# Kernel optimization log

Hardware: AMD Instinct MI355X
Metric: run time of the kernel (lower is better)

The kernel has to match this reference:

```python
import jax, jax.numpy as jnp
import numpy as np


def _phi(z, conv_w, conv_b):
    # z: (H, W, S, 1) -> 3x3 SAME conv over state channels -> softmax over states
    x = jnp.transpose(z[..., 0], (2, 0, 1))[None]  # (1, S, H, W)
    y = jax.lax.conv_general_dilated(
        x, conv_w, window_strides=(1, 1), padding='SAME',
        dimension_numbers=('NCHW', 'OIHW', 'NCHW')) + conv_b[None, :, None, None]
    return jax.nn.softmax(jnp.transpose(y[0], (1, 2, 0)), axis=2)[..., None]  # (H, W, S, 1)


def _update(obs, P, u_k, w_k_O, conv_w, conv_b):
    H, W, O = obs.shape
    S = P.shape[0]
    # b = P^T @ obs per cell: b[h,w,s] = sum_o P[o,s] * obs[h,w,o]
    b = jnp.einsum('os,hwo->hws', P, obs)[..., None]  # (H, W, S, 1)
    # Analytic Jacobian db/dP: deriv_b[h,w,s,0,i,j] = obs[h,w,i] * delta(s==j)
    eye = jnp.eye(S, O, dtype=obs.dtype)
    deriv_b = (obs[:, :, None, :, None] * eye[None, None, :, None, :])[:, :, :, None, :, :]  # (H,W,S,1,S,O)

    Bu = b * u_k                                  # (H, W, S, 1)
    bu = jnp.sum(Bu, axis=2, keepdims=True)       # (H, W, 1, 1)
    Z = Bu / bu                                   # Bu / bu

    u_kp1 = _phi(Z, conv_w, conv_b)               # (H, W, S, 1)

    # Sensitivity recursion for obs params (quotient rule on Bu/bu)
    du = deriv_b * u_k[..., None, None] + b[..., None, None] * w_k_O  # (H,W,S,1,S,O)
    term1 = du * bu[..., None, None]
    term2 = jnp.expand_dims(jnp.sum(du, axis=2), 3) * Bu[..., None, None]
    w_pre = (term1 - term2) / bu[..., None, None] ** 2                # (H,W,S,1,S,O)

    # J @ w  ==  9 JVPs of Phi at Z with tangent columns of w (exact, avoids dense (HWS)^2 Jacobian)
    tangents = jnp.moveaxis(w_pre.reshape(H, W, S, 1, S * O), -1, 0)  # (S*O, H, W, S, 1)
    jvp1 = lambda t: jax.jvp(lambda z: _phi(z, conv_w, conv_b), (Z,), (t,))[1]
    w_kp1_O = jnp.moveaxis(jax.vmap(jvp1)(tangents), 0, -1).reshape(H, W, S, 1, S, O)
    return u_kp1, w_kp1_O


def setup_inputs() -> dict:
    key = jax.random.key(0)
    k1, k2, k3 = jax.random.split(key, 3)
    H = W = 512
    S = O = 3
    obs = jax.random.uniform(k1, (H, W, O), dtype=jnp.float32)
    obs_param_matrix = jnp.ones((S, O), jnp.float32) / O          # row-stochastic init
    u_k = jnp.ones((H, W, S, 1), jnp.float32) / S                 # uniform belief
    w_k_O = jnp.zeros((H, W, S, 1, S, O), jnp.float32)
    conv_w = jax.random.normal(k2, (S, S, 3, 3), jnp.float32) * 0.1
    conv_b = jax.random.normal(k3, (S,), jnp.float32) * 0.1
    return {'obs': obs, 'obs_param_matrix': obs_param_matrix, 'u_k': u_k,
            'w_k_O': w_k_O, 'conv_w': conv_w, 'conv_b': conv_b}


def reference(obs, obs_param_matrix, u_k, w_k_O, conv_w, conv_b):
    return _update(obs, obs_param_matrix, u_k, w_k_O, conv_w, conv_b)
```

## Files before the change

kernel.cpp:

```cpp
#include <hip/hip_runtime.h>

#define IMH 512
#define IMW 512
#define TW 16
#define TH 16
#define HW_ (TW + 2)
#define HH_ (TH + 2)
#define NHALO (HW_ * HH_)
#define ROW 31

typedef float f4 __attribute__((ext_vector_type(4)));
typedef float f4a __attribute__((ext_vector_type(4), aligned(4)));
typedef float f2a __attribute__((ext_vector_type(2), aligned(4)));

__global__ __launch_bounds__(256, 4)
void hmm_fused(const float* __restrict__ obs,
               const float* __restrict__ P,
               const float* __restrict__ u_k,
               const float* __restrict__ w_k,
               const float* __restrict__ conv_w,
               const float* __restrict__ conv_b,
               float* __restrict__ out) {
    __shared__ __align__(16) float lds[NHALO * ROW];

    const int tid = threadIdx.x;
    const int w0 = blockIdx.x * TW;
    const int h0 = blockIdx.y * TH;

    float Pm[9];
#pragma unroll
    for (int i = 0; i < 9; ++i) Pm[i] = P[i];

    for (int p = tid; p < NHALO; p += 256) {
        const int hh = h0 + p / HW_ - 1;
        const int ww = w0 + p % HW_ - 1;
        float* row = &lds[p * ROW];
        if (hh < 0 || hh >= IMH || ww < 0 || ww >= IMW) {
#pragma unroll
            for (int c = 0; c < 30; ++c) row[c] = 0.0f;
            continue;
        }
        const int pix = hh * IMW + ww;

        const f2a o01 = *(const f2a*)(obs + pix * 3);
        const float o2 = obs[pix * 3 + 2];
        const f2a u01 = *(const f2a*)(u_k + pix * 3);
        const float u2 = u_k[pix * 3 + 2];
        const float ov[3] = {o01.x, o01.y, o2};
        const float us[3] = {u01.x, u01.y, u2};

        const float* wkp = &w_k[(size_t)pix * 27];
        float wreg[27];
        {
            const f4a* v4 = (const f4a*)wkp;
            const f4a a0 = v4[0], a1 = v4[1], a2 = v4[2], a3 = v4[3], a4 = v4[4], a5 = v4[5];
            const f2a a6 = *(const f2a*)(wkp + 24);
            const float a7 = wkp[26];
            wreg[0] = a0.x;  wreg[1] = a0.y;  wreg[2] = a0.z;  wreg[3] = a0.w;
            wreg[4] = a1.x;  wreg[5] = a1.y;  wreg[6] = a1.z;  wreg[7] = a1.w;
            wreg[8] = a2.x;  wreg[9] = a2.y;  wreg[10] = a2.z; wreg[11] = a2.w;
            wreg[12] = a3.x; wreg[13] = a3.y; wreg[14] = a3.z; wreg[15] = a3.w;
            wreg[16] = a4.x; wreg[17] = a4.y; wreg[18] = a4.z; wreg[19] = a4.w;
            wreg[20] = a5.x; wreg[21] = a5.y; wreg[22] = a5.z; wreg[23] = a5.w;
            wreg[24] = a6.x; wreg[25] = a6.y; wreg[26] = a7;
        }

        float b[3], Bu[3], bu = 0.0f;
#pragma unroll
        for (int s = 0; s < 3; ++s) {
            b[s] = Pm[0 * 3 + s] * ov[0] + Pm[1 * 3 + s] * ov[1] + Pm[2 * 3 + s] * ov[2];
            Bu[s] = b[s] * us[s];
            bu += Bu[s];
        }
        const float inv_bu = 1.0f / bu;
        float Z[3];
#pragma unroll
        for (int s = 0; s < 3; ++s) { Z[s] = Bu[s] * inv_bu; row[s] = Z[s]; }

#pragma unroll
        for (int i = 0; i < 3; ++i) {
#pragma unroll
            for (int j = 0; j < 3; ++j) {
                const int ij = i * 3 + j;
                float du[3], sdu = 0.0f;
#pragma unroll
                for (int s = 0; s < 3; ++s) {
                    float d = b[s] * wreg[s * 9 + ij];
                    if (s == j) d += ov[i] * us[s];
                    du[s] = d;
                    sdu += d;
                }
#pragma unroll
                for (int s = 0; s < 3; ++s)
                    row[(1 + ij) * 3 + s] = (du[s] - sdu * Z[s]) * inv_bu;
            }
        }
    }

    float cw[81];
#pragma unroll
    for (int i = 0; i < 81; ++i) cw[i] = conv_w[i];
    const float cb[3] = {conv_b[0], conv_b[1], conv_b[2]};

    __syncthreads();

    const int tx = tid % TW, ty = tid / TW;
    const int hp = (ty + 1) * HW_ + (tx + 1);
    const int pix = (h0 + ty) * IMW + (w0 + tx);

    float p0, p1, p2;
    {
        float y[3] = {cb[0], cb[1], cb[2]};
#pragma unroll
        for (int ky = 0; ky < 3; ++ky) {
#pragma unroll
            for (int kx = 0; kx < 3; ++kx) {
                const float* nb = &lds[(hp + (ky - 1) * HW_ + (kx - 1)) * ROW];
                const float v0 = nb[0], v1 = nb[1], v2 = nb[2];
#pragma unroll
                for (int s = 0; s < 3; ++s)
                    y[s] += cw[s * 27 + 0 * 9 + ky * 3 + kx] * v0 +
                            cw[s * 27 + 1 * 9 + ky * 3 + kx] * v1 +
                            cw[s * 27 + 2 * 9 + ky * 3 + kx] * v2;
            }
        }
        const float m = fmaxf(y[0], fmaxf(y[1], y[2]));
        const float e0 = __expf(y[0] - m), e1 = __expf(y[1] - m), e2 = __expf(y[2] - m);
        const float inv = 1.0f / (e0 + e1 + e2);
        p0 = e0 * inv; p1 = e1 * inv; p2 = e2 * inv;
        out[pix * 3 + 0] = p0; out[pix * 3 + 1] = p1; out[pix * 3 + 2] = p2;
    }

    float wout[27];
#pragma unroll
    for (int g = 1; g < 10; ++g) {
        float a[3] = {0.0f, 0.0f, 0.0f};
#pragma unroll
        for (int ky = 0; ky < 3; ++ky) {
#pragma unroll
            for (int kx = 0; kx < 3; ++kx) {
                const float* nb = &lds[(hp + (ky - 1) * HW_ + (kx - 1)) * ROW];
                const float v0 = nb[g * 3 + 0], v1 = nb[g * 3 + 1], v2 = nb[g * 3 + 2];
#pragma unroll
                for (int s = 0; s < 3; ++s)
                    a[s] += cw[s * 27 + 0 * 9 + ky * 3 + kx] * v0 +
                            cw[s * 27 + 1 * 9 + ky * 3 + kx] * v1 +
                            cw[s * 27 + 2 * 9 + ky * 3 + kx] * v2;
            }
        }
        const float dot = p0 * a[0] + p1 * a[1] + p2 * a[2];
        const int ij = g - 1;
        wout[0 * 9 + ij] = p0 * (a[0] - dot);
        wout[1 * 9 + ij] = p0 * 0.0f + p0 * (a[0] - dot);
        wout[0 * 9 + ij] = p0 * (a[0] - dot);
        wout[1 * 9 + ij] = p1 * (a[1] - dot);
        wout[2 * 9 + ij] = p2 * (a[2] - dot);
    }

    __syncthreads();

#pragma unroll
    for (int c = 0; c < 27; ++c) lds[tid * 27 + c] = wout[c];
    __syncthreads();

    const f4* lds4 = (const f4*)lds;
    float* outw = out + IMH * IMW * 3;
    for (int idx = tid; idx < TW * TH * 27 / 4; idx += 256) {
        const int r = idx / 108;
        const int rem = idx - r * 108;
        *(f4*)(&outw[(h0 + r) * (IMW * 27) + w0 * 27 + rem * 4]) = lds4[idx];
    }
}

extern "C" void kernel_launch(void* const* d_in, const int* in_sizes, int n_in,
                              void* d_out, int out_size, void* d_ws, size_t ws_size,
                              hipStream_t stream) {
    const float* obs    = (const float*)d_in[0];
    const float* P      = (const float*)d_in[1];
    const float* u_k    = (const float*)d_in[2];
    const float* w_k    = (const float*)d_in[3];
    const float* conv_w = (const float*)d_in[4];
    const float* conv_b = (const float*)d_in[5];
    float* out = (float*)d_out;

    dim3 grid(IMW / TW, IMH / TH);
    hmm_fused<<<grid, 256, 0, stream>>>(obs, P, u_k, w_k, conv_w, conv_b, out);
}
```

Before: 118.3 us.

## Halve tile height and split per-pixel tangent columns across two threads

Tiles shrink from 16x16 to 16x8 pixels while blocks keep 256 threads. The halo (180 cells) is now computed with one cell per thread, with no loop. For the second conv, two threads share each pixel: one handles 4 of the 9 tangent columns and the other handles 5. Both threads recompute the softmax. This halves LDS use and the per-thread register arrays, and the launch bound rises to 6 blocks per CU so occupancy and the number of blocks can grow. The costs are a larger halo-to-interior ratio, redundant softmax work, and an uneven 4/5 split between the two halves.

```diff
diff --git a/kernel.cpp b/kernel.cpp
--- a/kernel.cpp
+++ b/kernel.cpp
@@ -3,17 +3,18 @@
 #define IMH 512
 #define IMW 512
 #define TW 16
-#define TH 16
+#define TH 8
 #define HW_ (TW + 2)
 #define HH_ (TH + 2)
 #define NHALO (HW_ * HH_)
+#define NPIX (TW * TH)
 #define ROW 31
 
 typedef float f4 __attribute__((ext_vector_type(4)));
 typedef float f4a __attribute__((ext_vector_type(4), aligned(4)));
 typedef float f2a __attribute__((ext_vector_type(2), aligned(4)));
 
-__global__ __launch_bounds__(256, 4)
+__global__ __launch_bounds__(256, 6)
 void hmm_fused(const float* __restrict__ obs,
                const float* __restrict__ P,
                const float* __restrict__ u_k,
@@ -31,68 +32,69 @@
 #pragma unroll
     for (int i = 0; i < 9; ++i) Pm[i] = P[i];
 
-    for (int p = tid; p < NHALO; p += 256) {
+    if (tid < NHALO) {
+        const int p = tid;
         const int hh = h0 + p / HW_ - 1;
         const int ww = w0 + p % HW_ - 1;
         float* row = &lds[p * ROW];
         if (hh < 0 || hh >= IMH || ww < 0 || ww >= IMW) {
 #pragma unroll
             for (int c = 0; c < 30; ++c) row[c] = 0.0f;
-            continue;
-        }
-        const int pix = hh * IMW + ww;
+        } else {
+            const int pix = hh * IMW + ww;
 
-        const f2a o01 = *(const f2a*)(obs + pix * 3);
-        const float o2 = obs[pix * 3 + 2];
-        const f2a u01 = *(const f2a*)(u_k + pix * 3);
-        const float u2 = u_k[pix * 3 + 2];
-        const float ov[3] = {o01.x, o01.y, o2};
-        const float us[3] = {u01.x, u01.y, u2};
+            const f2a o01 = *(const f2a*)(obs + pix * 3);
+            const float o2 = obs[pix * 3 + 2];
+            const f2a u01 = *(const f2a*)(u_k + pix * 3);
+            const float u2 = u_k[pix * 3 + 2];
+            const float ov[3] = {o01.x, o01.y, o2};
+            const float us[3] = {u01.x, u01.y, u2};
 
-        const float* wkp = &w_k[(size_t)pix * 27];
-        float wreg[27];
-        {
-            const f4a* v4 = (const f4a*)wkp;
-            const f4a a0 = v4[0], a1 = v4[1], a2 = v4[2], a3 = v4[3], a4 = v4[4], a5 = v4[5];
-            const f2a a6 = *(const f2a*)(wkp + 24);
-            const float a7 = wkp[26];
-            wreg[0] = a0.x;  wreg[1] = a0.y;  wreg[2] = a0.z;  wreg[3] = a0.w;
-            wreg[4] = a1.x;  wreg[5] = a1.y;  wreg[6] = a1.z;  wreg[7] = a1.w;
-            wreg[8] = a2.x;  wreg[9] = a2.y;  wreg[10] = a2.z; wreg[11] = a2.w;
-            wreg[12] = a3.x; wreg[13] = a3.y; wreg[14] = a3.z; wreg[15] = a3.w;
-            wreg[16] = a4.x; wreg[17] = a4.y; wreg[18] = a4.z; wreg[19] = a4.w;
-            wreg[20] = a5.x; wreg[21] = a5.y; wreg[22] = a5.z; wreg[23] = a5.w;
-            wreg[24] = a6.x; wreg[25] = a6.y; wreg[26] = a7;
-        }
+            const float* wkp = &w_k[(size_t)pix * 27];
+            float wreg[27];
+            {
+                const f4a* v4 = (const f4a*)wkp;
+                const f4a a0 = v4[0], a1 = v4[1], a2 = v4[2], a3 = v4[3], a4 = v4[4], a5 = v4[5];
+                const f2a a6 = *(const f2a*)(wkp + 24);
+                const float a7 = wkp[26];
+                wreg[0] = a0.x;  wreg[1] = a0.y;  wreg[2] = a0.z;  wreg[3] = a0.w;
+                wreg[4] = a1.x;  wreg[5] = a1.y;  wreg[6] = a1.z;  wreg[7] = a1.w;
+                wreg[8] = a2.x;  wreg[9] = a2.y;  wreg[10] = a2.z; wreg[11] = a2.w;
+                wreg[12] = a3.x; wreg[13] = a3.y; wreg[14] = a3.z; wreg[15] = a3.w;
+                wreg[16] = a4.x; wreg[17] = a4.y; wreg[18] = a4.z; wreg[19] = a4.w;
+                wreg[20] = a5.x; wreg[21] = a5.y; wreg[22] = a5.z; wreg[23] = a5.w;
+                wreg[24] = a6.x; wreg[25] = a6.y; wreg[26] = a7;
+            }
 
-        float b[3], Bu[3], bu = 0.0f;
+            float b[3], Bu[3], bu = 0.0f;
 #pragma unroll
-        for (int s = 0; s < 3; ++s) {
-            b[s] = Pm[0 * 3 + s] * ov[0] + Pm[1 * 3 + s] * ov[1] + Pm[2 * 3 + s] * ov[2];
-            Bu[s] = b[s] * us[s];
-            bu += Bu[s];
-        }
-        const float inv_bu = 1.0f / bu;
-        float Z[3];
+            for (int s = 0; s < 3; ++s) {
+                b[s] = Pm[0 * 3 + s] * ov[0] + Pm[1 * 3 + s] * ov[1] + Pm[2 * 3 + s] * ov[2];
+                Bu[s] = b[s] * us[s];
+                bu += Bu[s];
+            }
+            const float inv_bu = 1.0f / bu;
+            float Z[3];
 #pragma unroll
-        for (int s = 0; s < 3; ++s) { Z[s] = Bu[s] * inv_bu; row[s] = Z[s]; }
+            for (int s = 0; s < 3; ++s) { Z[s] = Bu[s] * inv_bu; row[s] = Z[s]; }
 
 #pragma unroll
-        for (int i = 0; i < 3; ++i) {
+            for (int i = 0; i < 3; ++i) {
 #pragma unroll
-            for (int j = 0; j < 3; ++j) {
-                const int ij = i * 3 + j;
-                float du[3], sdu = 0.0f;
+                for (int j = 0; j < 3; ++j) {
+                    const int ij = i * 3 + j;
+                    float du[3], sdu = 0.0f;
 #pragma unroll
-                for (int s = 0; s < 3; ++s) {
-                    float d = b[s] * wreg[s * 9 + ij];
-                    if (s == j) d += ov[i] * us[s];
-                    du[s] = d;
-                    sdu += d;
+                    for (int s = 0; s < 3; ++s) {
+                        float d = b[s] * wreg[s * 9 + ij];
+                        if (s == j) d += ov[i] * us[s];
+                        du[s] = d;
+                        sdu += d;
+                    }
+#pragma unroll
+                    for (int s = 0; s < 3; ++s)
+                        row[(1 + ij) * 3 + s] = (du[s] - sdu * Z[s]) * inv_bu;
                 }
-#pragma unroll
-                for (int s = 0; s < 3; ++s)
-                    row[(1 + ij) * 3 + s] = (du[s] - sdu * Z[s]) * inv_bu;
             }
         }
     }
@@ -104,7 +106,9 @@
 
     __syncthreads();
 
-    const int tx = tid % TW, ty = tid / TW;
+    const int half = tid >> 7;
+    const int pxl = tid & 127;
+    const int tx = pxl & 15, ty = pxl >> 4;
     const int hp = (ty + 1) * HW_ + (tx + 1);
     const int pix = (h0 + ty) * IMW + (w0 + tx);
 
@@ -128,12 +132,16 @@
         const float e0 = __expf(y[0] - m), e1 = __expf(y[1] - m), e2 = __expf(y[2] - m);
         const float inv = 1.0f / (e0 + e1 + e2);
         p0 = e0 * inv; p1 = e1 * inv; p2 = e2 * inv;
-        out[pix * 3 + 0] = p0; out[pix * 3 + 1] = p1; out[pix * 3 + 2] = p2;
+        if (half == 0) { out[pix * 3 + 0] = p0; out[pix * 3 + 1] = p1; out[pix * 3 + 2] = p2; }
     }
 
-    float wout[27];
+    const int ij0 = half ? 4 : 0;
+    const int ng  = half ? 5 : 4;
+    float wout[5][3];
 #pragma unroll
-    for (int g = 1; g < 10; ++g) {
+    for (int k = 0; k < 5; ++k) {
+        if (k >= ng) break;
+        const int g = ij0 + k + 1;
         float a[3] = {0.0f, 0.0f, 0.0f};
 #pragma unroll
         for (int ky = 0; ky < 3; ++ky) {
@@ -149,23 +157,25 @@
             }
         }
         const float dot = p0 * a[0] + p1 * a[1] + p2 * a[2];
-        const int ij = g - 1;
-        wout[0 * 9 + ij] = p0 * (a[0] - dot);
-        wout[1 * 9 + ij] = p0 * 0.0f + p0 * (a[0] - dot);
-        wout[0 * 9 + ij] = p0 * (a[0] - dot);
-        wout[1 * 9 + ij] = p1 * (a[1] - dot);
-        wout[2 * 9 + ij] = p2 * (a[2] - dot);
+        wout[k][0] = p0 * (a[0] - dot);
+        wout[k][1] = p1 * (a[1] - dot);
+        wout[k][2] = p2 * (a[2] - dot);
     }
 
     __syncthreads();
 
 #pragma unroll
-    for (int c = 0; c < 27; ++c) lds[tid * 27 + c] = wout[c];
+    for (int k = 0; k < 5; ++k) {
+        if (k >= ng) break;
+        const int ij = ij0 + k;
+#pragma unroll
+        for (int s = 0; s < 3; ++s) lds[pxl * 27 + s * 9 + ij] = wout[k][s];
+    }
     __syncthreads();
 
     const f4* lds4 = (const f4*)lds;
     float* outw = out + IMH * IMW * 3;
-    for (int idx = tid; idx < TW * TH * 27 / 4; idx += 256) {
+    for (int idx = tid; idx < NPIX * 27 / 4; idx += 256) {
         const int r = idx / 108;
         const int rem = idx - r * 108;
         *(f4*)(&outw[(h0 + r) * (IMW * 27) + w0 * 27 + rem * 4]) = lds4[idx];
```

Result: slower. 145.9 us (+23.3%).

## Halve tile height and redistribute tangent convolution across threads by channel group

Applied to the files above, without the earlier changes.

Tile height drops to 8, so each 256-thread block loads its 180-pixel halo in a single pass. Softmax probabilities go to shared memory, and the nine tangent-channel convolutions are spread over 144 threads. Each of these threads owns one column and one channel group, sweeps down the rows with a rolling three-row accumulator, and writes results straight to global memory. This removes the per-thread 27-output serial loop and the LDS staging pass for output. In exchange, the output writes are strided rather than coalesced float4, and many threads sit idle in some phases.

```diff
diff --git a/kernel.cpp b/kernel.cpp
--- a/kernel.cpp
+++ b/kernel.cpp
@@ -3,10 +3,11 @@
 #define IMH 512
 #define IMW 512
 #define TW 16
-#define TH 16
+#define TH 8
 #define HW_ (TW + 2)
 #define HH_ (TH + 2)
 #define NHALO (HW_ * HH_)
+#define NPIX (TW * TH)
 #define ROW 31
 
 typedef float f4 __attribute__((ext_vector_type(4)));
@@ -22,6 +23,7 @@
                const float* __restrict__ conv_b,
                float* __restrict__ out) {
     __shared__ __align__(16) float lds[NHALO * ROW];
+    __shared__ f4 p_aux4[NPIX];
 
     const int tid = threadIdx.x;
     const int w0 = blockIdx.x * TW;
@@ -31,68 +33,69 @@
 #pragma unroll
     for (int i = 0; i < 9; ++i) Pm[i] = P[i];
 
-    for (int p = tid; p < NHALO; p += 256) {
+    if (tid < NHALO) {
+        const int p = tid;
         const int hh = h0 + p / HW_ - 1;
         const int ww = w0 + p % HW_ - 1;
         float* row = &lds[p * ROW];
         if (hh < 0 || hh >= IMH || ww < 0 || ww >= IMW) {
 #pragma unroll
             for (int c = 0; c < 30; ++c) row[c] = 0.0f;
-            continue;
-        }
-        const int pix = hh * IMW + ww;
-
-        const f2a o01 = *(const f2a*)(obs + pix * 3);
-        const float o2 = obs[pix * 3 + 2];
-        const f2a u01 = *(const f2a*)(u_k + pix * 3);
-        const float u2 = u_k[pix * 3 + 2];
-        const float ov[3] = {o01.x, o01.y, o2};
-        const float us[3] = {u01.x, u01.y, u2};
-
-        const float* wkp = &w_k[(size_t)pix * 27];
-        float wreg[27];
-        {
-            const f4a* v4 = (const f4a*)wkp;
-            const f4a a0 = v4[0], a1 = v4[1], a2 = v4[2], a3 = v4[3], a4 = v4[4], a5 = v4[5];
-            const f2a a6 = *(const f2a*)(wkp + 24);
-            const float a7 = wkp[26];
-            wreg[0] = a0.x;  wreg[1] = a0.y;  wreg[2] = a0.z;  wreg[3] = a0.w;
-            wreg[4] = a1.x;  wreg[5] = a1.y;  wreg[6] = a1.z;  wreg[7] = a1.w;
-            wreg[8] = a2.x;  wreg[9] = a2.y;  wreg[10] = a2.z; wreg[11] = a2.w;
-            wreg[12] = a3.x; wreg[13] = a3.y; wreg[14] = a3.z; wreg[15] = a3.w;
-            wreg[16] = a4.x; wreg[17] = a4.y; wreg[18] = a4.z; wreg[19] = a4.w;
-            wreg[20] = a5.x; wreg[21] = a5.y; wreg[22] = a5.z; wreg[23] = a5.w;
-            wreg[24] = a6.x; wreg[25] = a6.y; wreg[26] = a7;
-        }
-
-        float b[3], Bu[3], bu = 0.0f;
-#pragma unroll
-        for (int s = 0; s < 3; ++s) {
-            b[s] = Pm[0 * 3 + s] * ov[0] + Pm[1 * 3 + s] * ov[1] + Pm[2 * 3 + s] * ov[2];
-            Bu[s] = b[s] * us[s];
-            bu += Bu[s];
-        }
-        const float inv_bu = 1.0f / bu;
-        float Z[3];
-#pragma unroll
-        for (int s = 0; s < 3; ++s) { Z[s] = Bu[s] * inv_bu; row[s] = Z[s]; }
-
-#pragma unroll
-        for (int i = 0; i < 3; ++i) {
-#pragma unroll
-            for (int j = 0; j < 3; ++j) {
-                const int ij = i * 3 + j;
-                float du[3], sdu = 0.0f;
-#pragma unroll
-                for (int s = 0; s < 3; ++s) {
-                    float d = b[s] * wreg[s * 9 + ij];
-                    if (s == j) d += ov[i] * us[s];
-                    du[s] = d;
-                    sdu += d;
+        } else {
+            const int pix = hh * IMW + ww;
+
+            const f2a o01 = *(const f2a*)(obs + pix * 3);
+            const float o2 = obs[pix * 3 + 2];
+            const f2a u01 = *(const f2a*)(u_k + pix * 3);
+            const float u2 = u_k[pix * 3 + 2];
+            const float ov[3] = {o01.x, o01.y, o2};
+            const float us[3] = {u01.x, u01.y, u2};
+
+            const float* wkp = &w_k[(size_t)pix * 27];
+            float wreg[27];
+            {
+                const f4a* v4 = (const f4a*)wkp;
+                const f4a a0 = v4[0], a1 = v4[1], a2 = v4[2], a3 = v4[3], a4 = v4[4], a5 = v4[5];
+                const f2a a6 = *(const f2a*)(wkp + 24);
+                const float a7 = wkp[26];
+                wreg[0] = a0.x;  wreg[1] = a0.y;  wreg[2] = a0.z;  wreg[3] = a0.w;
+                wreg[4] = a1.x;  wreg[5] = a1.y;  wreg[6] = a1.z;  wreg[7] = a1.w;
+                wreg[8] = a2.x;  wreg[9] = a2.y;  wreg[10] = a2.z; wreg[11] = a2.w;
+                wreg[12] = a3.x; wreg[13] = a3.y; wreg[14] = a3.z; wreg[15] = a3.w;
+                wreg[16] = a4.x; wreg[17] = a4.y; wreg[18] = a4.z; wreg[19] = a4.w;
+                wreg[20] = a5.x; wreg[21] = a5.y; wreg[22] = a5.z; wreg[23] = a5.w;
+                wreg[24] = a6.x; wreg[25] = a6.y; wreg[26] = a7;
+            }
+
+            float b[3], Bu[3], bu = 0.0f;
+#pragma unroll
+            for (int s = 0; s < 3; ++s) {
+                b[s] = Pm[0 * 3 + s] * ov[0] + Pm[1 * 3 + s] * ov[1] + Pm[2 * 3 + s] * ov[2];
+                Bu[s] = b[s] * us[s];
+                bu += Bu[s];
+            }
+            const float inv_bu = 1.0f / bu;
+            float Z[3];
+#pragma unroll
+            for (int s = 0; s < 3; ++s) { Z[s] = Bu[s] * inv_bu; row[s] = Z[s]; }
+
+#pragma unroll
+            for (int i = 0; i < 3; ++i) {
+#pragma unroll
+                for (int j = 0; j < 3; ++j) {
+                    const int ij = i * 3 + j;
+                    float du[3], sdu = 0.0f;
+#pragma unroll
+                    for (int s = 0; s < 3; ++s) {
+                        float d = b[s] * wreg[s * 9 + ij];
+                        if (s == j) d += ov[i] * us[s];
+                        du[s] = d;
+                        sdu += d;
+                    }
+#pragma unroll
+                    for (int s = 0; s < 3; ++s)
+                        row[(1 + ij) * 3 + s] = (du[s] - sdu * Z[s]) * inv_bu;
                 }
-#pragma unroll
-                for (int s = 0; s < 3; ++s)
-                    row[(1 + ij) * 3 + s] = (du[s] - sdu * Z[s]) * inv_bu;
             }
         }
     }
@@ -100,75 +103,91 @@
     float cw[81];
 #pragma unroll
     for (int i = 0; i < 81; ++i) cw[i] = conv_w[i];
-    const float cb[3] = {conv_b[0], conv_b[1], conv_b[2]};
+    const float cb0 = conv_b[0], cb1 = conv_b[1], cb2 = conv_b[2];
 
     __syncthreads();
 
-    const int tx = tid % TW, ty = tid / TW;
-    const int hp = (ty + 1) * HW_ + (tx + 1);
-    const int pix = (h0 + ty) * IMW + (w0 + tx);
-
-    float p0, p1, p2;
-    {
-        float y[3] = {cb[0], cb[1], cb[2]};
+    float* outw = out + IMH * IMW * 3;
+
+    if (tid < NPIX) {
+        const int tx = tid & 15, ty = tid >> 4;
+        const int hp = (ty + 1) * HW_ + (tx + 1);
+        const int pix = (h0 + ty) * IMW + (w0 + tx);
+        float y0 = cb0, y1 = cb1, y2 = cb2;
 #pragma unroll
         for (int ky = 0; ky < 3; ++ky) {
 #pragma unroll
             for (int kx = 0; kx < 3; ++kx) {
                 const float* nb = &lds[(hp + (ky - 1) * HW_ + (kx - 1)) * ROW];
                 const float v0 = nb[0], v1 = nb[1], v2 = nb[2];
-#pragma unroll
-                for (int s = 0; s < 3; ++s)
-                    y[s] += cw[s * 27 + 0 * 9 + ky * 3 + kx] * v0 +
-                            cw[s * 27 + 1 * 9 + ky * 3 + kx] * v1 +
-                            cw[s * 27 + 2 * 9 + ky * 3 + kx] * v2;
+                const int T = ky * 3 + kx;
+                y0 += cw[0 + T] * v0 + cw[9 + T] * v1 + cw[18 + T] * v2;
+                y1 += cw[27 + T] * v0 + cw[36 + T] * v1 + cw[45 + T] * v2;
+                y2 += cw[54 + T] * v0 + cw[63 + T] * v1 + cw[72 + T] * v2;
             }
         }
-        const float m = fmaxf(y[0], fmaxf(y[1], y[2]));
-        const float e0 = __expf(y[0] - m), e1 = __expf(y[1] - m), e2 = __expf(y[2] - m);
+        const float m = fmaxf(y0, fmaxf(y1, y2));
+        const float e0 = __expf(y0 - m), e1 = __expf(y1 - m), e2 = __expf(y2 - m);
         const float inv = 1.0f / (e0 + e1 + e2);
-        p0 = e0 * inv; p1 = e1 * inv; p2 = e2 * inv;
+        const float p0 = e0 * inv, p1 = e1 * inv, p2 = e2 * inv;
         out[pix * 3 + 0] = p0; out[pix * 3 + 1] = p1; out[pix * 3 + 2] = p2;
+        p_aux4[tid] = (f4){p0, p1, p2, 0.0f};
     }
 
-    float wout[27];
-#pragma unroll
-    for (int g = 1; g < 10; ++g) {
-        float a[3] = {0.0f, 0.0f, 0.0f};
-#pragma unroll
-        for (int ky = 0; ky < 3; ++ky) {
-#pragma unroll
-            for (int kx = 0; kx < 3; ++kx) {
-                const float* nb = &lds[(hp + (ky - 1) * HW_ + (kx - 1)) * ROW];
-                const float v0 = nb[g * 3 + 0], v1 = nb[g * 3 + 1], v2 = nb[g * 3 + 2];
-#pragma unroll
-                for (int s = 0; s < 3; ++s)
-                    a[s] += cw[s * 27 + 0 * 9 + ky * 3 + kx] * v0 +
-                            cw[s * 27 + 1 * 9 + ky * 3 + kx] * v1 +
-                            cw[s * 27 + 2 * 9 + ky * 3 + kx] * v2;
-            }
-        }
-        const float dot = p0 * a[0] + p1 * a[1] + p2 * a[2];
+    __syncthreads();
+
+    if (tid < 144) {
+        const int x = tid & 15;
+        const int g = (tid >> 4) + 1;
         const int ij = g - 1;
-        wout[0 * 9 + ij] = p0 * (a[0] - dot);
-        wout[1 * 9 + ij] = p0 * 0.0f + p0 * (a[0] - dot);
-        wout[0 * 9 + ij] = p0 * (a[0] - dot);
-        wout[1 * 9 + ij] = p1 * (a[1] - dot);
-        wout[2 * 9 + ij] = p2 * (a[2] - dot);
-    }
-
-    __syncthreads();
-
-#pragma unroll
-    for (int c = 0; c < 27; ++c) lds[tid * 27 + c] = wout[c];
-    __syncthreads();
-
-    const f4* lds4 = (const f4*)lds;
-    float* outw = out + IMH * IMW * 3;
-    for (int idx = tid; idx < TW * TH * 27 / 4; idx += 256) {
-        const int r = idx / 108;
-        const int rem = idx - r * 108;
-        *(f4*)(&outw[(h0 + r) * (IMW * 27) + w0 * 27 + rem * 4]) = lds4[idx];
+        const int gch = 3 * g;
+
+        float a00, a01, a02;
+        float b10, b11, b12;
+        float c20, c21, c22;
+
+#define ROWFMA(P0_, P1_, P2_, KY)                                                        \
+        P0_ += cw[0 + (KY)*3 + 0] * v00 + cw[9 + (KY)*3 + 0] * v01 + cw[18 + (KY)*3 + 0] * v02; \
+        P1_ += cw[27 + (KY)*3 + 0] * v00 + cw[36 + (KY)*3 + 0] * v01 + cw[45 + (KY)*3 + 0] * v02; \
+        P2_ += cw[54 + (KY)*3 + 0] * v00 + cw[63 + (KY)*3 + 0] * v01 + cw[72 + (KY)*3 + 0] * v02; \
+        P0_ += cw[0 + (KY)*3 + 1] * v10 + cw[9 + (KY)*3 + 1] * v11 + cw[18 + (KY)*3 + 1] * v12; \
+        P1_ += cw[27 + (KY)*3 + 1] * v10 + cw[36 + (KY)*3 + 1] * v11 + cw[45 + (KY)*3 + 1] * v12; \
+        P2_ += cw[54 + (KY)*3 + 1] * v10 + cw[63 + (KY)*3 + 1] * v11 + cw[72 + (KY)*3 + 1] * v12; \
+        P0_ += cw[0 + (KY)*3 + 2] * v20 + cw[9 + (KY)*3 + 2] * v21 + cw[18 + (KY)*3 + 2] * v22; \
+        P1_ += cw[27 + (KY)*3 + 2] * v20 + cw[36 + (KY)*3 + 2] * v21 + cw[45 + (KY)*3 + 2] * v22; \
+        P2_ += cw[54 + (KY)*3 + 2] * v20 + cw[63 + (KY)*3 + 2] * v21 + cw[72 + (KY)*3 + 2] * v22;
+
+#define FINISH(O, Q0, Q1, Q2) {                                                          \
+        const f4 pv = p_aux4[(O) * 16 + x];                                              \
+        const float dot_ = pv.x * (Q0) + pv.y * (Q1) + pv.z * (Q2);                      \
+        float* wp = outw + ((size_t)((h0 + (O)) * IMW + (w0 + x))) * 27 + ij;            \
+        wp[0]  = pv.x * ((Q0) - dot_);                                                   \
+        wp[9]  = pv.y * ((Q1) - dot_);                                                   \
+        wp[18] = pv.z * ((Q2) - dot_); }
+
+#define STEP(R, N0,N1,N2, M0,M1,M2, O0,O1,O2, DO_N, DO_M, DO_O) {                        \
+        const int rb = ((R) * HW_ + x) * ROW + gch;                                      \
+        const float v00 = lds[rb + 0],  v01 = lds[rb + 1],  v02 = lds[rb + 2];           \
+        const float v10 = lds[rb + 31], v11 = lds[rb + 32], v12 = lds[rb + 33];          \
+        const float v20 = lds[rb + 62], v21 = lds[rb + 63], v22 = lds[rb + 64];          \
+        if (DO_N) { N0 = 0.0f; N1 = 0.0f; N2 = 0.0f; ROWFMA(N0, N1, N2, 0) }             \
+        if (DO_M) { ROWFMA(M0, M1, M2, 1) }                                              \
+        if (DO_O) { ROWFMA(O0, O1, O2, 2) FINISH((R) - 2, O0, O1, O2) } }
+
+        STEP(0, a00,a01,a02, b10,b11,b12, c20,c21,c22, true,  false, false)
+        STEP(1, b10,b11,b12, a00,a01,a02, c20,c21,c22, true,  true,  false)
+        STEP(2, c20,c21,c22, b10,b11,b12, a00,a01,a02, true,  true,  true )
+        STEP(3, a00,a01,a02, c20,c21,c22, b10,b11,b12, true,  true,  true )
+        STEP(4, b10,b11,b12, a00,a01,a02, c20,c21,c22, true,  true,  true )
+        STEP(5, c20,c21,c22, b10,b11,b12, a00,a01,a02, true,  true,  true )
+        STEP(6, a00,a01,a02, c20,c21,c22, b10,b11,b12, true,  true,  true )
+        STEP(7, b10,b11,b12, a00,a01,a02, c20,c21,c22, true,  true,  true )
+        STEP(8, c20,c21,c22, b10,b11,b12, a00,a01,a02, false, true,  true )
+        STEP(9, a00,a01,a02, c20,c21,c22, b10,b11,b12, false, false, true )
+
+#undef STEP
+#undef FINISH
+#undef ROWFMA
     }
 }
 
```

After: 105.6 us. -10.8%, faster.

## Split fused kernel into two stages via padded channel-planar workspace

Applied to the files above, without the earlier changes.

Replaces the single tiled kernel, which staged a haloed 30-channel tile in LDS, with two kernels. The first writes Z and the nine tangent groups into a zero-padded, channel-planar global workspace. The second reads 3x3 neighbourhoods straight from global memory and splits the nine JVP groups across two half-blocks. This removes LDS pressure, the halo recomputation and the barriers, at the cost of an extra round trip of about 30 MB through global memory and uncoalesced stride-27 output stores.

```diff
diff --git a/kernel.cpp b/kernel.cpp
--- a/kernel.cpp
+++ b/kernel.cpp
@@ -2,174 +2,155 @@
 
 #define IMH 512
 #define IMW 512
-#define TW 16
-#define TH 16
-#define HW_ (TW + 2)
-#define HH_ (TH + 2)
-#define NHALO (HW_ * HH_)
-#define ROW 31
+#define PW 514
+#define PS (PW * PW)
+#define NCH 30
+#define UOFF (IMH * IMW * 3)
 
-typedef float f4 __attribute__((ext_vector_type(4)));
 typedef float f4a __attribute__((ext_vector_type(4), aligned(4)));
 typedef float f2a __attribute__((ext_vector_type(2), aligned(4)));
 
+
 __global__ __launch_bounds__(256, 4)
-void hmm_fused(const float* __restrict__ obs,
-               const float* __restrict__ P,
-               const float* __restrict__ u_k,
-               const float* __restrict__ w_k,
-               const float* __restrict__ conv_w,
-               const float* __restrict__ conv_b,
-               float* __restrict__ out) {
-    __shared__ __align__(16) float lds[NHALO * ROW];
+void hmm_stage_a(const float* __restrict__ obs,
+                 const float* __restrict__ P,
+                 const float* __restrict__ u_k,
+                 const float* __restrict__ w_k,
+                 float* __restrict__ ws) {
+    const int cell = blockIdx.x * 256 + threadIdx.x;
+    if (cell >= PS) return;
+    const int y = cell / PW;
+    const int x = cell - y * PW;
 
-    const int tid = threadIdx.x;
-    const int w0 = blockIdx.x * TW;
-    const int h0 = blockIdx.y * TH;
+    if (y == 0 || y == PW - 1 || x == 0 || x == PW - 1) {
+#pragma unroll
+        for (int c = 0; c < NCH; ++c) ws[c * PS + cell] = 0.0f;
+        return;
+    }
 
     float Pm[9];
 #pragma unroll
     for (int i = 0; i < 9; ++i) Pm[i] = P[i];
 
-    for (int p = tid; p < NHALO; p += 256) {
-        const int hh = h0 + p / HW_ - 1;
-        const int ww = w0 + p % HW_ - 1;
-        float* row = &lds[p * ROW];
-        if (hh < 0 || hh >= IMH || ww < 0 || ww >= IMW) {
+    const int pix = (y - 1) * IMW + (x - 1);
+
+    const f2a o01 = *(const f2a*)(obs + pix * 3);
+    const float o2 = obs[pix * 3 + 2];
+    const f2a u01 = *(const f2a*)(u_k + pix * 3);
+    const float u2 = u_k[pix * 3 + 2];
+    const float ov[3] = {o01.x, o01.y, o2};
+    const float us[3] = {u01.x, u01.y, u2};
+
+    const float* wkp = &w_k[(size_t)pix * 27];
+    float wreg[27];
+    {
+        const f4a* v4 = (const f4a*)wkp;
+        const f4a a0 = v4[0], a1 = v4[1], a2 = v4[2], a3 = v4[3], a4 = v4[4], a5 = v4[5];
+        const f2a a6 = *(const f2a*)(wkp + 24);
+        const float a7 = wkp[26];
+        wreg[0] = a0.x;  wreg[1] = a0.y;  wreg[2] = a0.z;  wreg[3] = a0.w;
+        wreg[4] = a1.x;  wreg[5] = a1.y;  wreg[6] = a1.z;  wreg[7] = a1.w;
+        wreg[8] = a2.x;  wreg[9] = a2.y;  wreg[10] = a2.z; wreg[11] = a2.w;
+        wreg[12] = a3.x; wreg[13] = a3.y; wreg[14] = a3.z; wreg[15] = a3.w;
+        wreg[16] = a4.x; wreg[17] = a4.y; wreg[18] = a4.z; wreg[19] = a4.w;
+        wreg[20] = a5.x; wreg[21] = a5.y; wreg[22] = a5.z; wreg[23] = a5.w;
+        wreg[24] = a6.x; wreg[25] = a6.y; wreg[26] = a7;
+    }
+
+    float b[3], Bu[3], bu = 0.0f;
 #pragma unroll
-            for (int c = 0; c < 30; ++c) row[c] = 0.0f;
-            continue;
-        }
-        const int pix = hh * IMW + ww;
-
-        const f2a o01 = *(const f2a*)(obs + pix * 3);
-        const float o2 = obs[pix * 3 + 2];
-        const f2a u01 = *(const f2a*)(u_k + pix * 3);
-        const float u2 = u_k[pix * 3 + 2];
-        const float ov[3] = {o01.x, o01.y, o2};
-        const float us[3] = {u01.x, u01.y, u2};
-
-        const float* wkp = &w_k[(size_t)pix * 27];
-        float wreg[27];
-        {
-            const f4a* v4 = (const f4a*)wkp;
-            const f4a a0 = v4[0], a1 = v4[1], a2 = v4[2], a3 = v4[3], a4 = v4[4], a5 = v4[5];
-            const f2a a6 = *(const f2a*)(wkp + 24);
-            const float a7 = wkp[26];
-            wreg[0] = a0.x;  wreg[1] = a0.y;  wreg[2] = a0.z;  wreg[3] = a0.w;
-            wreg[4] = a1.x;  wreg[5] = a1.y;  wreg[6] = a1.z;  wreg[7] = a1.w;
-            wreg[8] = a2.x;  wreg[9] = a2.y;  wreg[10] = a2.z; wreg[11] = a2.w;
-            wreg[12] = a3.x; wreg[13] = a3.y; wreg[14] = a3.z; wreg[15] = a3.w;
-            wreg[16] = a4.x; wreg[17] = a4.y; wreg[18] = a4.z; wreg[19] = a4.w;
-            wreg[20] = a5.x; wreg[21] = a5.y; wreg[22] = a5.z; wreg[23] = a5.w;
-            wreg[24] = a6.x; wreg[25] = a6.y; wreg[26] = a7;
-        }
-
-        float b[3], Bu[3], bu = 0.0f;
+    for (int s = 0; s < 3; ++s) {
+        b[s] = Pm[0 * 3 + s] * ov[0] + Pm[1 * 3 + s] * ov[1] + Pm[2 * 3 + s] * ov[2];
+        Bu[s] = b[s] * us[s];
+        bu += Bu[s];
+    }
+    const float inv_bu = 1.0f / bu;
+    float Z[3];
 #pragma unroll
-        for (int s = 0; s < 3; ++s) {
-            b[s] = Pm[0 * 3 + s] * ov[0] + Pm[1 * 3 + s] * ov[1] + Pm[2 * 3 + s] * ov[2];
-            Bu[s] = b[s] * us[s];
-            bu += Bu[s];
-        }
-        const float inv_bu = 1.0f / bu;
-        float Z[3];
-#pragma unroll
-        for (int s = 0; s < 3; ++s) { Z[s] = Bu[s] * inv_bu; row[s] = Z[s]; }
+    for (int s = 0; s < 3; ++s) { Z[s] = Bu[s] * inv_bu; ws[s * PS + cell] = Z[s]; }
 
 #pragma unroll
-        for (int i = 0; i < 3; ++i) {
+    for (int i = 0; i < 3; ++i) {
 #pragma unroll
-            for (int j = 0; j < 3; ++j) {
-                const int ij = i * 3 + j;
-                float du[3], sdu = 0.0f;
+        for (int j = 0; j < 3; ++j) {
+            const int ij = i * 3 + j;
+            float du[3], sdu = 0.0f;
 #pragma unroll
-                for (int s = 0; s < 3; ++s) {
-                    float d = b[s] * wreg[s * 9 + ij];
-                    if (s == j) d += ov[i] * us[s];
-                    du[s] = d;
-                    sdu += d;
-                }
+            for (int s = 0; s < 3; ++s) {
+                float d = b[s] * wreg[s * 9 + ij];
+                if (s == j) d += ov[i] * us[s];
+                du[s] = d;
+                sdu += d;
+            }
 #pragma unroll
-                for (int s = 0; s < 3; ++s)
-                    row[(1 + ij) * 3 + s] = (du[s] - sdu * Z[s]) * inv_bu;
-            }
+            for (int s = 0; s < 3; ++s)
+                ws[((1 + ij) * 3 + s) * PS + cell] = (du[s] - sdu * Z[s]) * inv_bu;
         }
     }
+}
+
+__global__ __launch_bounds__(256, 4)
+void hmm_stage_b(const float* __restrict__ ws,
+                 const float* __restrict__ conv_w,
+                 const float* __restrict__ conv_b,
+                 float* __restrict__ out) {
+    const int tid = threadIdx.x;
+    const int half = tid >> 7;
+    const int pix = blockIdx.x * 128 + (tid & 127);
+    const int h = pix >> 9, w = pix & 511;
+    const int base = (h + 1) * PW + (w + 1);
 
     float cw[81];
 #pragma unroll
     for (int i = 0; i < 81; ++i) cw[i] = conv_w[i];
-    const float cb[3] = {conv_b[0], conv_b[1], conv_b[2]};
+    const float cb0 = conv_b[0], cb1 = conv_b[1], cb2 = conv_b[2];
 
-    __syncthreads();
-
-    const int tx = tid % TW, ty = tid / TW;
-    const int hp = (ty + 1) * HW_ + (tx + 1);
-    const int pix = (h0 + ty) * IMW + (w0 + tx);
-
-    float p0, p1, p2;
-    {
-        float y[3] = {cb[0], cb[1], cb[2]};
-#pragma unroll
-        for (int ky = 0; ky < 3; ++ky) {
-#pragma unroll
-            for (int kx = 0; kx < 3; ++kx) {
-                const float* nb = &lds[(hp + (ky - 1) * HW_ + (kx - 1)) * ROW];
-                const float v0 = nb[0], v1 = nb[1], v2 = nb[2];
-#pragma unroll
-                for (int s = 0; s < 3; ++s)
-                    y[s] += cw[s * 27 + 0 * 9 + ky * 3 + kx] * v0 +
-                            cw[s * 27 + 1 * 9 + ky * 3 + kx] * v1 +
-                            cw[s * 27 + 2 * 9 + ky * 3 + kx] * v2;
-            }
-        }
-        const float m = fmaxf(y[0], fmaxf(y[1], y[2]));
-        const float e0 = __expf(y[0] - m), e1 = __expf(y[1] - m), e2 = __expf(y[2] - m);
-        const float inv = 1.0f / (e0 + e1 + e2);
-        p0 = e0 * inv; p1 = e1 * inv; p2 = e2 * inv;
-        out[pix * 3 + 0] = p0; out[pix * 3 + 1] = p1; out[pix * 3 + 2] = p2;
+#define GCONV(G, A0, A1, A2)                                                      \
+    {                                                                             \
+        const float* q0 = ws + (3 * (G) + 0) * PS + base;                         \
+        const float* q1 = ws + (3 * (G) + 1) * PS + base;                         \
+        const float* q2 = ws + (3 * (G) + 2) * PS + base;                         \
+        _Pragma("unroll")                                                         \
+        for (int dy = -1; dy <= 1; ++dy) {                                        \
+            _Pragma("unroll")                                                     \
+            for (int dx = -1; dx <= 1; ++dx) {                                    \
+                const int off = dy * PW + dx;                                     \
+                const int T = (dy + 1) * 3 + (dx + 1);                            \
+                const float v0 = q0[off], v1 = q1[off], v2 = q2[off];             \
+                A0 += cw[0 + T] * v0 + cw[9 + T] * v1 + cw[18 + T] * v2;          \
+                A1 += cw[27 + T] * v0 + cw[36 + T] * v1 + cw[45 + T] * v2;        \
+                A2 += cw[54 + T] * v0 + cw[63 + T] * v1 + cw[72 + T] * v2;        \
+            }                                                                     \
+        }                                                                         \
     }
 
-    float wout[27];
-#pragma unroll
-    for (int g = 1; g < 10; ++g) {
-        float a[3] = {0.0f, 0.0f, 0.0f};
-#pragma unroll
-        for (int ky = 0; ky < 3; ++ky) {
-#pragma unroll
-            for (int kx = 0; kx < 3; ++kx) {
-                const float* nb = &lds[(hp + (ky - 1) * HW_ + (kx - 1)) * ROW];
-                const float v0 = nb[g * 3 + 0], v1 = nb[g * 3 + 1], v2 = nb[g * 3 + 2];
-#pragma unroll
-                for (int s = 0; s < 3; ++s)
-                    a[s] += cw[s * 27 + 0 * 9 + ky * 3 + kx] * v0 +
-                            cw[s * 27 + 1 * 9 + ky * 3 + kx] * v1 +
-                            cw[s * 27 + 2 * 9 + ky * 3 + kx] * v2;
-            }
-        }
-        const float dot = p0 * a[0] + p1 * a[1] + p2 * a[2];
-        const int ij = g - 1;
-        wout[0 * 9 + ij] = p0 * (a[0] - dot);
-        wout[1 * 9 + ij] = p0 * 0.0f + p0 * (a[0] - dot);
-        wout[0 * 9 + ij] = p0 * (a[0] - dot);
-        wout[1 * 9 + ij] = p1 * (a[1] - dot);
-        wout[2 * 9 + ij] = p2 * (a[2] - dot);
+    float y0 = cb0, y1 = cb1, y2 = cb2;
+    GCONV(0, y0, y1, y2)
+    const float m = fmaxf(y0, fmaxf(y1, y2));
+    const float e0 = __expf(y0 - m), e1 = __expf(y1 - m), e2 = __expf(y2 - m);
+    const float inv = 1.0f / (e0 + e1 + e2);
+    const float p0 = e0 * inv, p1 = e1 * inv, p2 = e2 * inv;
+
+    float* wp = out + UOFF + (size_t)pix * 27;
+
+#define GROUP_JVP(G, IJ)                                                          \
+    {                                                                             \
+        float a0 = 0.0f, a1 = 0.0f, a2 = 0.0f;                                    \
+        GCONV(G, a0, a1, a2)                                                      \
+        const float dot_ = p0 * a0 + p1 * a1 + p2 * a2;                           \
+        wp[(IJ) + 0]  = p0 * (a0 - dot_);                                         \
+        wp[(IJ) + 9]  = p1 * (a1 - dot_);                                         \
+        wp[(IJ) + 18] = p2 * (a2 - dot_);                                         \
     }
 
-    __syncthreads();
-
-#pragma unroll
-    for (int c = 0; c < 27; ++c) lds[tid * 27 + c] = wout[c];
-    __syncthreads();
-
-    const f4* lds4 = (const f4*)lds;
-    float* outw = out + IMH * IMW * 3;
-    for (int idx = tid; idx < TW * TH * 27 / 4; idx += 256) {
-        const int r = idx / 108;
-        const int rem = idx - r * 108;
-        *(f4*)(&outw[(h0 + r) * (IMW * 27) + w0 * 27 + rem * 4]) = lds4[idx];
+    if (half == 0) {
+        out[pix * 3 + 0] = p0; out[pix * 3 + 1] = p1; out[pix * 3 + 2] = p2;
+        GROUP_JVP(1, 0) GROUP_JVP(2, 1) GROUP_JVP(3, 2) GROUP_JVP(4, 3)
+    } else {
+        GROUP_JVP(5, 4) GROUP_JVP(6, 5) GROUP_JVP(7, 6) GROUP_JVP(8, 7) GROUP_JVP(9, 8)
     }
+#undef GROUP_JVP
+#undef GCONV
 }
 
 extern "C" void kernel_launch(void* const* d_in, const int* in_sizes, int n_in,
@@ -182,7 +163,11 @@
     const float* conv_w = (const float*)d_in[4];
     const float* conv_b = (const float*)d_in[5];
     float* out = (float*)d_out;
+    float* ws  = (float*)d_ws;
 
-    dim3 grid(IMW / TW, IMH / TH);
-    hmm_fused<<<grid, 256, 0, stream>>>(obs, P, u_k, w_k, conv_w, conv_b, out);
+    const int blocksA = (PS + 255) / 256;
+    hmm_stage_a<<<blocksA, 256, 0, stream>>>(obs, P, u_k, w_k, ws);
+
+    const int blocksB = (IMH * IMW) / 128;
+    hmm_stage_b<<<blocksB, 256, 0, stream>>>(ws, conv_w, conv_b, out);
 }
```

Result: slower. 127.5 us (+7.7%).
